# Performance work log

Hardware: AMD Instinct MI355X
Metric: run time of the kernel (lower is better)

The kernel has to match this reference:

```python
import jax, jax.numpy as jnp
import numpy as np

D_MODEL = 1024
NUM_HEADS = 16


def setup_inputs() -> dict:
    key = jax.random.key(0)
    ks = jax.random.split(key, 11)
    B, S, D = 2, 2048, D_MODEL
    s = 1.0 / np.sqrt(D)
    return {
        "queries": jax.random.normal(ks[0], (B, S, D), jnp.float32),
        "keys": jax.random.normal(ks[1], (B, S, D), jnp.float32),
        "values": jax.random.normal(ks[2], (B, S, D), jnp.float32),
        "W_q": jax.random.normal(ks[3], (D, D), jnp.float32) * s,
        "b_q": jnp.zeros((D,), jnp.float32),
        "W_k": jax.random.normal(ks[4], (D, D), jnp.float32) * s,
        "b_k": jnp.zeros((D,), jnp.float32),
        "W_v": jax.random.normal(ks[5], (D, D), jnp.float32) * s,
        "b_v": jnp.zeros((D,), jnp.float32),
        "W_o": jax.random.normal(ks[6], (D, D), jnp.float32) * s,
        "b_o": jnp.zeros((D,), jnp.float32),
    }


def _split_heads(x, num_heads):
    # [B, S, D] -> [B, H, S, d_h]
    B, S, D = x.shape
    return x.reshape(B, S, num_heads, D // num_heads).transpose(0, 2, 1, 3)


def reference(queries, keys, values, W_q, b_q, W_k, b_k, W_v, b_v, W_o, b_o):
    H = NUM_HEADS
    Q = _split_heads(queries @ W_q.T + b_q, H)  # [B,H,S,dh]
    K = _split_heads(keys @ W_k.T + b_k, H)
    V = _split_heads(values @ W_v.T + b_v, H)
    d = Q.shape[-1]
    scores = jnp.einsum("bhqd,bhkd->bhqk", Q, K) / jnp.sqrt(jnp.asarray(d, Q.dtype))
    attn = jax.nn.softmax(scores, axis=-1)
    out = jnp.einsum("bhqk,bhkd->bhqd", attn, V)  # [B,H,S,dh]
    B, _, S, _ = out.shape
    out = out.transpose(0, 2, 1, 3).reshape(B, S, -1)  # combine heads
    return out @ W_o.T + b_o
```

## Files before the change

### kernel.cpp

```cpp
#include <hip/hip_runtime.h>
#include <cstdint>
#include <cmath>

typedef short s16x8 __attribute__((ext_vector_type(8)));
typedef short s16x4 __attribute__((ext_vector_type(4)));
typedef float f32x4 __attribute__((ext_vector_type(4)));
typedef unsigned int u32;

#define AS_G __attribute__((address_space(1)))
#define AS_L __attribute__((address_space(3)))

#define QSCALE 0.18033688011112042f

__device__ __forceinline__ void ld16_to_lds(const void* g, const void* l) {
    __builtin_amdgcn_global_load_lds((AS_G void*)(g), (AS_L void*)(l), 16, 0, 0);
}

__device__ __forceinline__ short f2bf(float f) {
    union { float f; uint32_t u; } v; v.f = f;
    uint32_t r = v.u + 0x7fffu + ((v.u >> 16) & 1u);
    return (short)(r >> 16);
}

template<int F32OUT, int NJ, int QKV>
__global__ __launch_bounds__(256, 3)
void gemm_bt(const short* __restrict__ Abase, long Az,
             const short* __restrict__ Wbase, long Wz,
             const float* __restrict__ bias0, const float* __restrict__ bias1,
             const float* __restrict__ bias2,
             void* __restrict__ Obase, long Oz,
             const int M, const int N, const int K)
{
    constexpr int BN = NJ * 32;
    constexpr int BSt = (BN * 4) / 256;
    constexpr int LPS = 2 + BSt;
    __shared__ __align__(16) short As[3][128 * 32];
    __shared__ __align__(16) short Bs[3][BN * 32];

    const int t = threadIdx.x, lane = t & 63, wv = t >> 6;
    const int wr = wv >> 1, wc = wv & 1;
    const int q4 = lane >> 4, l16 = lane & 15;

    const u32 gx = gridDim.x, gy = gridDim.y;
    u32 lin = blockIdx.x + gx * (blockIdx.y + gy * blockIdx.z);
    const u32 nwg = gx * gy * gridDim.z;
    if ((nwg & 7u) == 0u) lin = (lin & 7u) * (nwg >> 3) + (lin >> 3);
    const int bxs = lin % gx;
    const u32 rem = lin / gx;
    const int bys = rem % gy;
    const int z   = rem / gy;

    const short* A  = Abase + (long)z * Az;
    const short* Bt = Wbase + (long)z * Wz;
    const float* bias = (z == 0) ? bias0 : ((z == 1) ? bias1 : bias2);
    const float bmul = (QKV && z == 0) ? QSCALE : 1.0f;
    const int bn0 = bxs * BN, bm0 = bys * 128;

    f32x4 acc[4][NJ] = {};

    const short* gA[2];
    const short* gB[BSt];
    #pragma unroll
    for (int s = 0; s < 2; ++s) {
        const int c = t + 256 * s;
        const int r = c >> 2, g = (c & 3) ^ ((c >> 3) & 3);
        gA[s] = A + (size_t)(bm0 + r) * K + g * 8;
    }
    #pragma unroll
    for (int s = 0; s < BSt; ++s) {
        const int c = t + 256 * s;
        const int r = c >> 2, g = (c & 3) ^ ((c >> 3) & 3);
        gB[s] = Bt + (size_t)(bn0 + r) * K + g * 8;
    }

    auto stage = [&](int buf) {
        #pragma unroll
        for (int s = 0; s < 2; ++s) {
            ld16_to_lds(gA[s], &As[buf][(wv * 64 + 256 * s) * 8]);
            gA[s] += 32;
        }
        #pragma unroll
        for (int s = 0; s < BSt; ++s) {
            ld16_to_lds(gB[s], &Bs[buf][(wv * 64 + 256 * s) * 8]);
            gB[s] += 32;
        }
    };

    const int kIters = K >> 5;
    stage(0);
    stage(1);
    for (int kt = 0; kt < kIters; ++kt) {
        const int cur = kt % 3;
        if (kt < kIters - 1)
            asm volatile("s_waitcnt vmcnt(%0)" :: "n"(LPS) : "memory");
        else
            asm volatile("s_waitcnt vmcnt(0)" ::: "memory");
        __builtin_amdgcn_s_barrier();
        __builtin_amdgcn_sched_barrier(0);
        if (kt + 2 < kIters) stage((kt + 2) % 3);

        s16x8 aF[4], bF[NJ];
        #pragma unroll
        for (int i = 0; i < 4; ++i) {
            const int m = wr * 64 + i * 16 + l16;
            aF[i] = *(const s16x8*)&As[cur][m * 32 + (q4 ^ ((m >> 1) & 3)) * 8];
        }
        #pragma unroll
        for (int j = 0; j < NJ; ++j) {
            const int n = wc * (BN / 2) + j * 16 + l16;
            bF[j] = *(const s16x8*)&Bs[cur][n * 32 + (q4 ^ ((n >> 1) & 3)) * 8];
        }
        #pragma unroll
        for (int i = 0; i < 4; ++i)
            #pragma unroll
            for (int j = 0; j < NJ; ++j)
                acc[i][j] = __builtin_amdgcn_mfma_f32_16x16x32_bf16(
                    aF[i], bF[j], acc[i][j], 0, 0, 0);
    }

    #pragma unroll
    for (int j = 0; j < NJ; ++j) {
        const int col = bn0 + wc * (BN / 2) + j * 16 + l16;
        const float bj = bias[col] * bmul;
        #pragma unroll
        for (int i = 0; i < 4; ++i) {
            const int row0 = bm0 + wr * 64 + i * 16 + q4 * 4;
            if (QKV && z == 2) {
                s16x4 ov;
                #pragma unroll
                for (int r = 0; r < 4; ++r) ov[r] = f2bf(acc[i][j][r] + bj);
                *(s16x4*)(((short*)Obase + (long)z * Oz) +
                          (size_t)col * 4096 + row0) = ov;
            } else {
                #pragma unroll
                for (int r = 0; r < 4; ++r) {
                    const float v = acc[i][j][r] + bj;
                    if (F32OUT)
                        ((float*)Obase + (long)z * Oz)[(size_t)(row0 + r) * N + col] = v;
                    else
                        ((short*)Obase + (long)z * Oz)[(size_t)(row0 + r) * N + col] = f2bf(v);
                }
            }
        }
    }
}

__global__ __launch_bounds__(256, 2)
void attn_fwd(const short* __restrict__ Qp, const short* __restrict__ Kp,
              const short* __restrict__ VpT, short* __restrict__ Out)
{
    constexpr int D = 1024, S = 2048;
    __shared__ __align__(16) short Ks[2][512 * 8];
    __shared__ __align__(16) short Vt[2][512 * 8];

    const int t = threadIdx.x, lane = t & 63, wv = t >> 6;
    const int q4 = lane >> 4, l16 = lane & 15;
    const int bid = blockIdx.x;
    const int qt = (bid >> 3) & 15;
    const int hb = (bid & 7) * 4 + (bid >> 7);
    const int h = hb >> 1, b = hb & 1;
    const size_t rowB = (size_t)b * S;
    const int cb = h * 64;
    const int qrow0 = qt * 128 + wv * 32;

    s16x8 qF[2][2];
    #pragma unroll
    for (int i = 0; i < 2; ++i)
        #pragma unroll
        for (int tk = 0; tk < 2; ++tk)
            qF[i][tk] = *(const s16x8*)
                &Qp[(rowB + qrow0 + i * 16 + l16) * D + cb + tk * 32 + q4 * 8];

    f32x4 oacc[2][4] = {};
    f32x4 lacc[2] = {};
    s16x8 onesF;
    #pragma unroll
    for (int e = 0; e < 8; ++e) onesF[e] = (short)0x3F80;

    const short* KpB = Kp + rowB * D + cb;
    const short* VtG = VpT + (size_t)cb * 4096 + b * 2048;

    auto stageKV = [&](int buf, int kv0) {
        #pragma unroll
        for (int s = 0; s < 2; ++s) {
            const int slot = (4 * s + wv) * 64 + lane;
            const int r = slot >> 3;
            const int kcs = (slot & 7) ^ (r & 7);
            ld16_to_lds(KpB + (size_t)(kv0 + r) * D + kcs * 8,
                        &Ks[buf][(wv * 64 + 256 * s) * 8]);
        }
        #pragma unroll
        for (int s = 0; s < 2; ++s) {
            const int c = t + 256 * s;
            const int d = c >> 3, kcp = c & 7;
            ld16_to_lds(VtG + (size_t)d * 4096 + kv0 + ((kcp ^ (d & 7)) * 8),
                        &Vt[buf][(wv * 64 + 256 * s) * 8]);
        }
    };

    stageKV(0, 0);

    for (int kvt = 0; kvt < 32; ++kvt) {
        const int kv0 = kvt * 64;
        __syncthreads();
        if (kvt < 31) stageKV((kvt + 1) & 1, kv0 + 64);

        f32x4 acc[2][4] = {};
        #pragma unroll
        for (int tk = 0; tk < 2; ++tk) {
            s16x8 kA[4];
            #pragma unroll
            for (int j = 0; j < 4; ++j)
                kA[j] = *(const s16x8*)
                    &Ks[kvt & 1][((j * 16 + l16) * 8 +
                                  ((tk * 4 + q4) ^ (l16 & 7))) * 8];
            #pragma unroll
            for (int j = 0; j < 4; ++j) {
                acc[0][j] = __builtin_amdgcn_mfma_f32_16x16x32_bf16(
                    kA[j], qF[0][tk], acc[0][j], 0, 0, 0);
                acc[1][j] = __builtin_amdgcn_mfma_f32_16x16x32_bf16(
                    kA[j], qF[1][tk], acc[1][j], 0, 0, 0);
            }
        }

        union { s16x8 v; u32 w[4]; } pA[2][2];
        #pragma unroll
        for (int i = 0; i < 2; ++i) {
            u32 cc[4][2];
            #pragma unroll
            for (int j = 0; j < 4; ++j) {
                const float p0 = __builtin_amdgcn_exp2f(acc[i][j][0]);
                const float p1 = __builtin_amdgcn_exp2f(acc[i][j][1]);
                const float p2 = __builtin_amdgcn_exp2f(acc[i][j][2]);
                const float p3 = __builtin_amdgcn_exp2f(acc[i][j][3]);
                asm("v_cvt_pk_bf16_f32 %0, %1, %2" : "=v"(cc[j][0]) : "v"(p0), "v"(p1));
                asm("v_cvt_pk_bf16_f32 %0, %1, %2" : "=v"(cc[j][1]) : "v"(p2), "v"(p3));
            }
            #pragma unroll
            for (int tkp = 0; tkp < 2; ++tkp)
                #pragma unroll
                for (int bb = 0; bb < 2; ++bb) {
                    u32 x = cc[2 * tkp][bb], y = cc[2 * tkp + 1][bb];
                    asm("v_permlane32_swap_b32 %0, %1" : "+v"(x), "+v"(y));
                    asm("v_permlane16_swap_b32 %0, %1" : "+v"(x), "+v"(y));
                    pA[i][tkp].w[bb] = x;
                    pA[i][tkp].w[2 + bb] = y;
                }
        }

        #pragma unroll
        for (int tkp = 0; tkp < 2; ++tkp) {
            lacc[0] = __builtin_amdgcn_mfma_f32_16x16x32_bf16(
                pA[0][tkp].v, onesF, lacc[0], 0, 0, 0);
            lacc[1] = __builtin_amdgcn_mfma_f32_16x16x32_bf16(
                pA[1][tkp].v, onesF, lacc[1], 0, 0, 0);
            #pragma unroll
            for (int jd = 0; jd < 4; ++jd) {
                const int d = jd * 16 + l16;
                const s16x8 vF = *(const s16x8*)
                    &Vt[kvt & 1][(d * 8 + ((tkp * 4 + q4) ^ (d & 7))) * 8];
                oacc[0][jd] = __builtin_amdgcn_mfma_f32_16x16x32_bf16(
                    pA[0][tkp].v, vF, oacc[0][jd], 0, 0, 0);
                oacc[1][jd] = __builtin_amdgcn_mfma_f32_16x16x32_bf16(
                    pA[1][tkp].v, vF, oacc[1][jd], 0, 0, 0);
            }
        }
    }

    #pragma unroll
    for (int i = 0; i < 2; ++i)
        #pragma unroll
        for (int r = 0; r < 4; ++r) {
            const float inv = 1.0f / lacc[i][r];
            const size_t row = rowB + qrow0 + i * 16 + q4 * 4 + r;
            #pragma unroll
            for (int jd = 0; jd < 4; ++jd)
                Out[row * D + cb + jd * 16 + l16] = f2bf(oacc[i][jd][r] * inv);
        }
}

__global__ __launch_bounds__(256)
void cast_all(const float* __restrict__ q, const float* __restrict__ k,
              const float* __restrict__ v, const float* __restrict__ wq,
              const float* __restrict__ wk, const float* __restrict__ wv,
              const float* __restrict__ wo, short* __restrict__ out)
{
    const size_t i = ((size_t)blockIdx.x * 256 + threadIdx.x) * 8;
    const float* src; size_t off;
    if      (i < 4194304)  { src = q;  off = i; }
    else if (i < 8388608)  { src = k;  off = i - 4194304; }
    else if (i < 12582912) { src = v;  off = i - 8388608; }
    else if (i < 13631488) { src = wq; off = i - 12582912; }
    else if (i < 14680064) { src = wk; off = i - 13631488; }
    else if (i < 15728640) { src = wv; off = i - 14680064; }
    else                   { src = wo; off = i - 15728640; }
    const float m = (i >= 12582912 && i < 13631488) ? QSCALE : 1.0f;
    const float4 a = *(const float4*)(src + off);
    const float4 c = *(const float4*)(src + off + 4);
    s16x8 o;
    o[0] = f2bf(a.x * m); o[1] = f2bf(a.y * m); o[2] = f2bf(a.z * m); o[3] = f2bf(a.w * m);
    o[4] = f2bf(c.x * m); o[5] = f2bf(c.y * m); o[6] = f2bf(c.z * m); o[7] = f2bf(c.w * m);
    *(s16x8*)(out + i) = o;
}

extern "C" void kernel_launch(void* const* d_in, const int* in_sizes, int n_in,
                              void* d_out, int out_size, void* d_ws, size_t ws_size,
                              hipStream_t stream)
{
    const float* q  = (const float*)d_in[0];
    const float* k  = (const float*)d_in[1];
    const float* v  = (const float*)d_in[2];
    const float* Wq = (const float*)d_in[3];
    const float* bq = (const float*)d_in[4];
    const float* Wk = (const float*)d_in[5];
    const float* bk = (const float*)d_in[6];
    const float* Wv = (const float*)d_in[7];
    const float* bv = (const float*)d_in[8];
    const float* Wo = (const float*)d_in[9];
    const float* bo = (const float*)d_in[10];

    short* ws = (short*)d_ws;
    const long MEL = 1048576;
    short* Aq  = ws;
    short* Wqb = ws + 12 * MEL;
    short* Wob = ws + 15 * MEL;
    short* Qp  = ws + 16 * MEL;
    short* Kp  = ws + 20 * MEL;
    short* VpT = ws + 24 * MEL;
    short* AO  = ws;

    cast_all<<<8192, 256, 0, stream>>>(q, k, v, Wq, Wk, Wv, Wo, ws);

    gemm_bt<0, 4, 1><<<dim3(8, 32, 3), 256, 0, stream>>>(
        Aq, 4 * MEL, Wqb, 1 * MEL, bq, bk, bv, Qp, 4 * MEL, 4096, 1024, 1024);

    attn_fwd<<<512, 256, 0, stream>>>(Qp, Kp, VpT, AO);

    gemm_bt<1, 2, 0><<<dim3(16, 32, 1), 256, 0, stream>>>(
        AO, 0, Wob, 0, bo, bo, bo, d_out, 0, 4096, 1024, 1024);
}
```

Before: 214.2 us.

## Switch GEMM to double-buffered BK=64 tiles with 8-way XOR swizzle

Replaces the 3-stage, K=32-per-step LDS pipeline with a 2-stage pipeline that stages 64 K-elements per step. Each step now runs two MFMA sub-steps, halving the number of barriers and K iterations. The LDS swizzle changes to an 8-chunk XOR pattern to match the wider rows, and the launch bound drops from 3 to 2 blocks per CU. The trade-off is a larger LDS footprint per block and less load-ahead depth, so there is less latency hiding in exchange for fewer synchronizations.

```diff
diff --git a/kernel.cpp b/kernel.cpp
--- a/kernel.cpp
+++ b/kernel.cpp
@@ -23,7 +23,7 @@
 }
 
 template<int F32OUT, int NJ, int QKV>
-__global__ __launch_bounds__(256, 3)
+__global__ __launch_bounds__(256, 2)
 void gemm_bt(const short* __restrict__ Abase, long Az,
              const short* __restrict__ Wbase, long Wz,
              const float* __restrict__ bias0, const float* __restrict__ bias1,
@@ -32,10 +32,10 @@
              const int M, const int N, const int K)
 {
     constexpr int BN = NJ * 32;
-    constexpr int BSt = (BN * 4) / 256;
-    constexpr int LPS = 2 + BSt;
-    __shared__ __align__(16) short As[3][128 * 32];
-    __shared__ __align__(16) short Bs[3][BN * 32];
+    constexpr int ASt = 4;
+    constexpr int BSt = (BN * 8) / 256;
+    __shared__ __align__(16) short As[2][128 * 64];
+    __shared__ __align__(16) short Bs[2][BN * 64];
 
     const int t = threadIdx.x, lane = t & 63, wv = t >> 6;
     const int wr = wv >> 1, wc = wv & 1;
@@ -58,64 +58,63 @@
 
     f32x4 acc[4][NJ] = {};
 
-    const short* gA[2];
+    const short* gA[ASt];
     const short* gB[BSt];
     #pragma unroll
-    for (int s = 0; s < 2; ++s) {
+    for (int s = 0; s < ASt; ++s) {
         const int c = t + 256 * s;
-        const int r = c >> 2, g = (c & 3) ^ ((c >> 3) & 3);
+        const int r = c >> 3, g = (c & 7) ^ (r & 7);
         gA[s] = A + (size_t)(bm0 + r) * K + g * 8;
     }
     #pragma unroll
     for (int s = 0; s < BSt; ++s) {
         const int c = t + 256 * s;
-        const int r = c >> 2, g = (c & 3) ^ ((c >> 3) & 3);
+        const int r = c >> 3, g = (c & 7) ^ (r & 7);
         gB[s] = Bt + (size_t)(bn0 + r) * K + g * 8;
     }
 
     auto stage = [&](int buf) {
         #pragma unroll
-        for (int s = 0; s < 2; ++s) {
+        for (int s = 0; s < ASt; ++s) {
             ld16_to_lds(gA[s], &As[buf][(wv * 64 + 256 * s) * 8]);
-            gA[s] += 32;
+            gA[s] += 64;
         }
         #pragma unroll
         for (int s = 0; s < BSt; ++s) {
             ld16_to_lds(gB[s], &Bs[buf][(wv * 64 + 256 * s) * 8]);
-            gB[s] += 32;
+            gB[s] += 64;
         }
     };
 
-    const int kIters = K >> 5;
+    const int kIters = K >> 6;
     stage(0);
-    stage(1);
     for (int kt = 0; kt < kIters; ++kt) {
-        const int cur = kt % 3;
-        if (kt < kIters - 1)
-            asm volatile("s_waitcnt vmcnt(%0)" :: "n"(LPS) : "memory");
-        else
-            asm volatile("s_waitcnt vmcnt(0)" ::: "memory");
-        __builtin_amdgcn_s_barrier();
-        __builtin_amdgcn_sched_barrier(0);
-        if (kt + 2 < kIters) stage((kt + 2) % 3);
-
-        s16x8 aF[4], bF[NJ];
-        #pragma unroll
-        for (int i = 0; i < 4; ++i) {
-            const int m = wr * 64 + i * 16 + l16;
-            aF[i] = *(const s16x8*)&As[cur][m * 32 + (q4 ^ ((m >> 1) & 3)) * 8];
-        }
-        #pragma unroll
-        for (int j = 0; j < NJ; ++j) {
-            const int n = wc * (BN / 2) + j * 16 + l16;
-            bF[j] = *(const s16x8*)&Bs[cur][n * 32 + (q4 ^ ((n >> 1) & 3)) * 8];
-        }
-        #pragma unroll
-        for (int i = 0; i < 4; ++i)
-            #pragma unroll
-            for (int j = 0; j < NJ; ++j)
-                acc[i][j] = __builtin_amdgcn_mfma_f32_16x16x32_bf16(
-                    aF[i], bF[j], acc[i][j], 0, 0, 0);
+        const int cur = kt & 1;
+        __syncthreads();
+        if (kt + 1 < kIters) stage(cur ^ 1);
+
+        #pragma unroll
+        for (int tk = 0; tk < 2; ++tk) {
+            s16x8 aF[4], bF[NJ];
+            #pragma unroll
+            for (int i = 0; i < 4; ++i) {
+                const int m = wr * 64 + i * 16 + l16;
+                aF[i] = *(const s16x8*)
+                    &As[cur][(m * 8 + ((tk * 4 + q4) ^ (m & 7))) * 8];
+            }
+            #pragma unroll
+            for (int j = 0; j < NJ; ++j) {
+                const int n = wc * (BN / 2) + j * 16 + l16;
+                bF[j] = *(const s16x8*)
+                    &Bs[cur][(n * 8 + ((tk * 4 + q4) ^ (n & 7))) * 8];
+            }
+            #pragma unroll
+            for (int i = 0; i < 4; ++i)
+                #pragma unroll
+                for (int j = 0; j < NJ; ++j)
+                    acc[i][j] = __builtin_amdgcn_mfma_f32_16x16x32_bf16(
+                        aF[i], bF[j], acc[i][j], 0, 0, 0);
+        }
     }
 
     #pragma unroll
```

New measurement: 219.4 us. +2.4%, slower.
